# Optimization experiments

Measured on AMD Instinct MI355X. Metric: run time of the kernel, lower is better.

## Reference

```python
import jax, jax.numpy as jnp
import numpy as np

L = 16384; ENC = 64; DMODEL = 256; DSTATE = 64; DCONV = 4; EXPAND = 2
NLAYERS = 3; NCLASSES = 11
DIN = EXPAND * DMODEL                 # 512
HEADDIM = 64
NHEADS = DIN // HEADDIM               # 8
DXBC = DIN + 2 * DSTATE               # 640 (ngroups=1)
DPROJ = 2 * DIN + 2 * DSTATE + NHEADS # 1160
NDIR = 6
ORDERS = [(0, 1, 2), (0, 2, 1), (1, 0, 2), (1, 2, 0), (2, 0, 1), (2, 1, 0)]
SCALES = [1, 2, 4]
EPS = 1e-5


def setup_inputs() -> dict:
    key = jax.random.key(0)
    ks = iter(jax.random.split(key, 64))
    def nrm(shape, s=0.02):
        return jax.random.normal(next(ks), shape, jnp.float32) * s
    S = len(SCALES)
    return {
        "vec_real": jax.random.normal(next(ks), (L, ENC), jnp.float32),
        "vec_imag": jax.random.normal(next(ks), (L, ENC), jnp.float32),
        "coords": jax.random.randint(next(ks), (L, 4), 0, 128, jnp.int32),
        # input projection (Linear 128->256, LayerNorm)
        "inp_w": nrm((2 * ENC, DMODEL)), "inp_b": jnp.zeros((DMODEL,)),
        "inp_ln_w": jnp.ones((DMODEL,)), "inp_ln_b": jnp.zeros((DMODEL,)),
        # shared Mamba2 blocks, stacked over NLAYERS
        "ln_w": jnp.ones((NLAYERS, DMODEL)), "ln_b": jnp.zeros((NLAYERS, DMODEL)),
        "in_proj_w": nrm((NLAYERS, DMODEL, DPROJ)),
        "conv_w": nrm((NLAYERS, DXBC, DCONV), 0.1), "conv_b": jnp.zeros((NLAYERS, DXBC)),
        "dt_bias": nrm((NLAYERS, NHEADS), 0.5),
        "A_log": jnp.log(jnp.broadcast_to(jnp.arange(1, NHEADS + 1, dtype=jnp.float32), (NLAYERS, NHEADS))),
        "Dskip": jnp.ones((NLAYERS, NHEADS)),
        "rms_w": jnp.ones((NLAYERS, DIN)),
        "out_proj_w": nrm((NLAYERS, DIN, DMODEL)),
        # fusion MLP
        "fus_ln_w": jnp.ones((NDIR * DMODEL,)), "fus_ln_b": jnp.zeros((NDIR * DMODEL,)),
        "fus_w": nrm((NDIR * DMODEL, DMODEL)), "fus_b": jnp.zeros((DMODEL,)),
        # classifier
        "cls_ln_w": jnp.ones((S * DMODEL,)), "cls_ln_b": jnp.zeros((S * DMODEL,)),
        "cls_w1": nrm((S * DMODEL, 2 * DMODEL)), "cls_b1": jnp.zeros((2 * DMODEL,)),
        "cls_w2": nrm((2 * DMODEL, DMODEL)), "cls_b2": jnp.zeros((DMODEL,)),
        "cls_w3": nrm((DMODEL, NCLASSES)), "cls_b3": jnp.zeros((NCLASSES,)),
    }


def layer_norm(x, w, b):
    mu = x.mean(-1, keepdims=True)
    v = ((x - mu) ** 2).mean(-1, keepdims=True)
    return (x - mu) * jax.lax.rsqrt(v + EPS) * w + b


def mamba2(x, in_proj_w, conv_w, conv_b, dt_bias, A_log, Dskip, rms_w, out_proj_w):
    # x: [B, L, DMODEL]
    Bsz, Ls, _ = x.shape
    zxbcdt = x @ in_proj_w                                  # [B,L,DPROJ]
    z, xBC, dt = jnp.split(zxbcdt, [DIN, DIN + DXBC], axis=-1)
    dt = jax.nn.softplus(dt + dt_bias)                      # [B,L,H]
    # causal depthwise conv1d over xBC, then SiLU
    xc = jnp.transpose(xBC, (0, 2, 1))                      # [B,C,L]
    xc = jax.lax.conv_general_dilated(xc, conv_w[:, None, :], (1,), [(DCONV - 1, 0)],
                                      feature_group_count=DXBC)
    xBC = jax.nn.silu(jnp.transpose(xc, (0, 2, 1)) + conv_b)
    xs, Bm, Cm = jnp.split(xBC, [DIN, DIN + DSTATE], axis=-1)
    xs = xs.reshape(Bsz, Ls, NHEADS, HEADDIM)               # [B,L,H,P]
    A = -jnp.exp(A_log)                                     # [H]

    def step(state, inp):
        x_t, B_t, C_t, dt_t = inp                           # [B,H,P],[B,S],[B,S],[B,H]
        dA = jnp.exp(dt_t * A)                              # [B,H]
        state = state * dA[..., None, None] + (dt_t[..., None, None]
                 * x_t[..., :, None] * B_t[:, None, None, :])
        y = jnp.einsum('bhps,bs->bhp', state, C_t)
        return state, y

    init = jnp.zeros((Bsz, NHEADS, HEADDIM, DSTATE), x.dtype)
    seq = (jnp.moveaxis(xs, 1, 0), jnp.moveaxis(Bm, 1, 0),
           jnp.moveaxis(Cm, 1, 0), jnp.moveaxis(dt, 1, 0))
    _, ys = jax.lax.scan(step, init, seq)                   # [L,B,H,P]
    y = jnp.moveaxis(ys, 0, 1) + Dskip[None, None, :, None] * xs
    y = y.reshape(Bsz, Ls, DIN)
    # gated RMSNorm (norm_before_gate=False)
    y = y * jax.nn.silu(z)
    y = y * jax.lax.rsqrt((y * y).mean(-1, keepdims=True) + EPS) * rms_w
    return y @ out_proj_w


def reference(vec_real, vec_imag, coords, inp_w, inp_b, inp_ln_w, inp_ln_b,
              ln_w, ln_b, in_proj_w, conv_w, conv_b, dt_bias, A_log, Dskip,
              rms_w, out_proj_w, fus_ln_w, fus_ln_b, fus_w, fus_b,
              cls_ln_w, cls_ln_b, cls_w1, cls_b1, cls_w2, cls_b2, cls_w3, cls_b3):
    x = jnp.concatenate([vec_real, vec_imag], -1)           # [L,128]
    h = layer_norm(x @ inp_w + inp_b, inp_ln_w, inp_ln_b)
    h = jax.nn.gelu(h, approximate=False)                   # [L,D]
    # 6 traversal orders via lexsort (np.lexsort semantics: last key primary)
    perms = [jnp.lexsort(tuple(coords[:, a] for a in reversed(axes))) for axes in ORDERS]
    perm = jnp.stack(perms)                                 # [6,L]
    inv = jnp.argsort(perm, axis=1)                         # [6,L]
    xs = h[perm]                                            # [6,L,D] (directions as batch, shared weights)

    def layer_step(xcur, p):
        lw, lb, ipw, cw, cb, dtb, al, dk, rw, ow = p
        y = mamba2(layer_norm(xcur, lw, lb), ipw, cw, cb, dtb, al, dk, rw, ow)
        return xcur + y, None

    params = (ln_w, ln_b, in_proj_w, conv_w, conv_b, dt_bias, A_log, Dskip, rms_w, out_proj_w)
    xs, _ = jax.lax.scan(layer_step, xs, params)
    restored = jnp.take_along_axis(xs, inv[:, :, None], axis=1)  # [6,L,D]
    multi = jnp.transpose(restored, (1, 0, 2)).reshape(L, NDIR * DMODEL)
    fused = layer_norm(multi, fus_ln_w, fus_ln_b) @ fus_w + fus_b
    fused = jax.nn.gelu(fused, approximate=False)           # [L,D]
    # multi-scale pooling; L divisible by every scale -> equal windows
    pooled = jnp.concatenate([fused.reshape(s, L // s, DMODEL).mean(1).mean(0)
                              for s in SCALES], 0)          # [3*D]
    hc = layer_norm(pooled, cls_ln_w, cls_ln_b)
    hc = jax.nn.gelu(hc @ cls_w1 + cls_b1, approximate=False)
    hc = jax.nn.gelu(hc @ cls_w2 + cls_b2, approximate=False)
    return hc @ cls_w3 + cls_b3                             # [NCLASSES]
```

## Files before the change

### kernel.cpp

```cpp
#include <hip/hip_runtime.h>
#include <hip/hip_bf16.h>
#include <math.h>

#define LSEQ 16384
#define NC 128

using short8  = __attribute__((ext_vector_type(8))) short;
using floatx4 = __attribute__((ext_vector_type(4))) float;

__device__ __forceinline__ float bf2f(ushort u){ union{unsigned u; float f;} x; x.u = ((unsigned)u)<<16; return x.f; }
__device__ __forceinline__ ushort f2bf(float f){ union{float f; unsigned u;} x; x.f=f; unsigned u=x.u; return (ushort)((u + 0x7FFFu + ((u>>16)&1u)) >> 16); }
__device__ __forceinline__ float geluf(float x){ return 0.5f*x*(1.f+erff(x*0.70710678118654752f)); }
__device__ __forceinline__ float siluf(float x){ return x/(1.f+__expf(-x)); }
__device__ __forceinline__ float softplusf(float x){ return x>20.f ? x : log1pf(__expf(x)); }

__device__ __forceinline__ float blockSum256(float v, float* red){
  int t = threadIdx.x;
  red[t]=v; __syncthreads();
  #pragma unroll
  for (int s=128;s>0;s>>=1){ if (t<s) red[t]+=red[t+s]; __syncthreads(); }
  float r = red[0]; __syncthreads();
  return r;
}

__device__ const int ORD[6][3] = {{0,1,2},{0,2,1},{1,0,2},{1,2,0},{2,0,1},{2,1,0}};

__global__ __launch_bounds__(256) void sort_k(const int* __restrict__ coords, int* __restrict__ perm, int* __restrict__ inv){
  __shared__ unsigned long long sk[256];
  int d = blockIdx.y; int tid = threadIdx.x;
  int a0=ORD[d][0], a1=ORD[d][1], a2=ORD[d][2];
  int ibase = blockIdx.x*1024;
  unsigned long long mykey[4]; int rank[4] = {0,0,0,0};
  #pragma unroll
  for (int r=0;r<4;++r){
    int i = ibase + r*256 + tid;
    unsigned k3 = ((unsigned)coords[i*4+a0]<<14) | ((unsigned)coords[i*4+a1]<<7) | (unsigned)coords[i*4+a2];
    mykey[r] = (((unsigned long long)k3)<<14) | (unsigned)i;
  }
  for (int j0=0; j0<LSEQ; j0+=256){
    int j = j0 + tid;
    unsigned j3 = ((unsigned)coords[j*4+a0]<<14) | ((unsigned)coords[j*4+a1]<<7) | (unsigned)coords[j*4+a2];
    sk[tid] = (((unsigned long long)j3)<<14) | (unsigned)j;
    __syncthreads();
    #pragma unroll 8
    for (int jj=0; jj<256; ++jj){
      unsigned long long kj = sk[jj];
      #pragma unroll
      for (int r=0;r<4;++r) rank[r] += (kj < mykey[r]) ? 1 : 0;
    }
    __syncthreads();
  }
  #pragma unroll
  for (int r=0;r<4;++r){
    int i = ibase + r*256 + tid;
    perm[d*LSEQ + rank[r]] = i;
    inv[d*LSEQ + i] = rank[r];
  }
}

__global__ __launch_bounds__(256) void concat_k(const float* __restrict__ vr, const float* __restrict__ vi, float* __restrict__ xcat){
  int idx = blockIdx.x*256 + threadIdx.x;
  int i = idx >> 7, c = idx & 127;
  xcat[idx] = (c<64) ? vr[(i<<6)+c] : vi[(i<<6)+c-64];
}

__global__ __launch_bounds__(256) void tr_k(const float* __restrict__ in, ushort* __restrict__ out, int K, int N){
  __shared__ float tile[32][33];
  int tx = threadIdx.x & 31, ty = threadIdx.x >> 5;
  int k0 = blockIdx.y*32, n0 = blockIdx.x*32;
  #pragma unroll
  for (int q=0;q<4;++q){
    int k = k0 + ty + q*8, n = n0 + tx;
    if (k < K && n < N) tile[ty+q*8][tx] = in[(size_t)k*N + n];
  }
  __syncthreads();
  #pragma unroll
  for (int q=0;q<4;++q){
    int n = n0 + ty + q*8, k = k0 + tx;
    if (n < N && k < K) out[(size_t)n*K + k] = f2bf(tile[tx][ty+q*8]);
  }
}

template<int EPI, bool AF32>
__global__ __launch_bounds__(256) void gemm_bf_k(
  const void* __restrict__ Ain, int lda, const ushort* __restrict__ Bt,
  int N, int K, float* __restrict__ of,
  const float* __restrict__ bias, const float* __restrict__ rrow)
{
  __shared__ __align__(16) ushort As[64*32];
  __shared__ __align__(16) ushort Bs[64*32];
  int tid = threadIdx.x;
  int n0 = blockIdx.x*64, m0 = blockIdx.y*64;
  int w = tid>>6, lane = tid&63;
  int wm = (w>>1)*32, wn = (w&1)*32;
  int sr = tid>>2, skk = (tid&3)*8;
  floatx4 acc[2][2] = {};
  for (int k0=0; k0<K; k0+=32){
    if constexpr (AF32){
      const float* A = (const float*)Ain;
      float4 v0 = *(const float4*)(A + (size_t)(m0+sr)*lda + k0 + skk);
      float4 v1 = *(const float4*)(A + (size_t)(m0+sr)*lda + k0 + skk + 4);
      ushort o[8] = {f2bf(v0.x),f2bf(v0.y),f2bf(v0.z),f2bf(v0.w),f2bf(v1.x),f2bf(v1.y),f2bf(v1.z),f2bf(v1.w)};
      *(uint4*)(&As[sr*32+skk]) = *(uint4*)o;
    } else {
      const ushort* A = (const ushort*)Ain;
      *(uint4*)(&As[sr*32+skk]) = *(const uint4*)(A + (size_t)(m0+sr)*lda + k0 + skk);
    }
    uint4 bv = make_uint4(0u,0u,0u,0u);
    if (n0+sr < N) bv = *(const uint4*)(Bt + (size_t)(n0+sr)*K + k0 + skk);
    *(uint4*)(&Bs[sr*32+skk]) = bv;
    __syncthreads();
    int kq = lane>>4, l16 = lane&15;
    short8 bf0 = *(const short8*)(&Bs[(wn      + l16)*32 + kq*8]);
    short8 bf1 = *(const short8*)(&Bs[(wn + 16 + l16)*32 + kq*8]);
    #pragma unroll
    for (int ti=0; ti<2; ++ti){
      short8 af = *(const short8*)(&As[(wm + ti*16 + l16)*32 + kq*8]);
      acc[ti][0] = __builtin_amdgcn_mfma_f32_16x16x32_bf16(af, bf0, acc[ti][0], 0,0,0);
      acc[ti][1] = __builtin_amdgcn_mfma_f32_16x16x32_bf16(af, bf1, acc[ti][1], 0,0,0);
    }
    __syncthreads();
  }
  int l16 = lane&15, lq = lane>>4;
  #pragma unroll
  for (int ti=0; ti<2; ++ti)
  #pragma unroll
  for (int tj=0; tj<2; ++tj)
  #pragma unroll
  for (int r=0; r<4; ++r){
    int row = m0 + wm + ti*16 + lq*4 + r;
    int col = n0 + wn + tj*16 + l16;
    if (col >= N) continue;
    float v = acc[ti][tj][r];
    if (EPI==0){ of[(size_t)row*N + col] = v + bias[col]; }
    else if (EPI==2){ of[(size_t)row*N + col] += v * rrow[row]; }
    else { of[(size_t)row*N + col] = geluf(v + bias[col]); }
  }
}

__global__ __launch_bounds__(256) void gemm1_k(
  const float* __restrict__ xs,
  const float* __restrict__ lnw, const float* __restrict__ lnb,
  const ushort* __restrict__ Wt,
  ushort* __restrict__ xbc, float* __restrict__ odt, const float* __restrict__ dtb)
{
  __shared__ __align__(16) ushort As[64*264];
  __shared__ __align__(16) ushort Bs[64*32];
  int tid = threadIdx.x;
  int m0 = blockIdx.x*64;
  int w = tid>>6, lane = tid&63;
  int wm = (w>>1)*32, wn = (w&1)*32;
  int sr = tid>>2, skk = (tid&3)*8;
  int l16 = lane&15, kq = lane>>4;
  float va[8][8];
  float s = 0.f, s2 = 0.f;
  const float* rowp = xs + (size_t)(m0+sr)*256;
  #pragma unroll
  for (int ki=0;ki<8;++ki){
    float4 v0 = *(const float4*)(rowp + ki*32 + skk);
    float4 v1 = *(const float4*)(rowp + ki*32 + skk + 4);
    va[ki][0]=v0.x; va[ki][1]=v0.y; va[ki][2]=v0.z; va[ki][3]=v0.w;
    va[ki][4]=v1.x; va[ki][5]=v1.y; va[ki][6]=v1.z; va[ki][7]=v1.w;
    #pragma unroll
    for (int j=0;j<8;++j){ s += va[ki][j]; s2 += va[ki][j]*va[ki][j]; }
  }
  s  += __shfl_xor(s,1,64);  s  += __shfl_xor(s,2,64);
  s2 += __shfl_xor(s2,1,64); s2 += __shfl_xor(s2,2,64);
  float mu = s*(1.f/256.f);
  float var = s2*(1.f/256.f) - mu*mu;
  float rs = rsqrtf(fmaxf(var,0.f)+1e-5f);
  #pragma unroll
  for (int ki=0;ki<8;++ki){
    ushort o[8];
    #pragma unroll
    for (int j=0;j<8;++j) o[j] = f2bf((va[ki][j]-mu)*rs*lnw[ki*32+skk+j] + lnb[ki*32+skk+j]);
    *(uint4*)(&As[sr*264 + ki*32 + skk]) = *(uint4*)o;
  }
  __syncthreads();
  for (int nt=0; nt<11; ++nt){
    floatx4 acc[2][2] = {};
    for (int k0=0; k0<256; k0+=32){
      int nr = 512 + nt*64 + sr;
      uint4 bv = make_uint4(0u,0u,0u,0u);
      if (nr < 1160) bv = *(const uint4*)(Wt + (size_t)nr*256 + k0 + skk);
      *(uint4*)(&Bs[sr*32+skk]) = bv;
      __syncthreads();
      short8 bf0 = *(const short8*)(&Bs[(wn      + l16)*32 + kq*8]);
      short8 bf1 = *(const short8*)(&Bs[(wn + 16 + l16)*32 + kq*8]);
      #pragma unroll
      for (int ti=0; ti<2; ++ti){
        short8 af = *(const short8*)(&As[(wm + ti*16 + l16)*264 + k0 + kq*8]);
        acc[ti][0] = __builtin_amdgcn_mfma_f32_16x16x32_bf16(af, bf0, acc[ti][0], 0,0,0);
        acc[ti][1] = __builtin_amdgcn_mfma_f32_16x16x32_bf16(af, bf1, acc[ti][1], 0,0,0);
      }
      __syncthreads();
    }
    #pragma unroll
    for (int ti=0; ti<2; ++ti)
    #pragma unroll
    for (int tj=0; tj<2; ++tj)
    #pragma unroll
    for (int r=0; r<4; ++r){
      int row = m0 + wm + ti*16 + kq*4 + r;
      int col = nt*64 + wn + tj*16 + l16;
      float v = acc[ti][tj][r];
      if (col < 640) xbc[(size_t)row*640 + col] = f2bf(v);
      else if (col < 648) odt[(size_t)row*8 + (col-640)] = softplusf(v + dtb[col-640]);
    }
  }
}

__global__ __launch_bounds__(256) void ln_gelu_k(const float* __restrict__ in, float* __restrict__ out,
    const float* __restrict__ w, const float* __restrict__ b){
  __shared__ float red[256];
  int t = threadIdx.x; size_t base = (size_t)blockIdx.x*256;
  float v = in[base+t];
  float mu = blockSum256(v, red) * (1.f/256.f);
  float dv = v - mu;
  float var = blockSum256(dv*dv, red) * (1.f/256.f);
  float rs = rsqrtf(var + 1e-5f);
  out[base+t] = geluf(dv*rs*w[t] + b[t]);
}

__global__ __launch_bounds__(256) void scatter_k(const float* __restrict__ h, const int* __restrict__ perm, float* __restrict__ xs){
  int blk = blockIdx.x;
  int t = threadIdx.x;
  int d = blk >> 14; int r = blk & 16383;
  int src = perm[d*LSEQ + r];
  xs[(size_t)blk*256 + t] = h[(size_t)src*256 + t];
}

__global__ __launch_bounds__(256) void bnd_k(const ushort* __restrict__ xbc, ushort* __restrict__ bnd){
  int b = blockIdx.x;
  int d = b / NC, c = b % NC;
  size_t row0 = (size_t)d*LSEQ + (size_t)c*128;
  for (int idx = threadIdx.x; idx < 3*640; idx += 256){
    int j = idx/640;
    ushort v = (c==0) ? (ushort)0 : xbc[(row0 - 3 + j)*640 + (idx - j*640)];
    bnd[(size_t)b*3*640 + idx] = v;
  }
}

__global__ __launch_bounds__(256) void conv_k(ushort* __restrict__ xbc, const ushort* __restrict__ bnd,
    const float* __restrict__ convw, const float* __restrict__ convb){
  int b = blockIdx.x;
  int d = b / NC, c = b % NC;
  size_t row0 = (size_t)d*LSEQ + (size_t)c*128;
  int tid = threadIdx.x;
  for (int s0 = tid; s0 < 640; s0 += 256){
    float w0=convw[s0*4], w1=convw[s0*4+1], w2=convw[s0*4+2], w3=convw[s0*4+3];
    float cb=convb[s0];
    float h0=0.f,h1=0.f,h2=0.f;
    if (c != 0){
      const ushort* bp = bnd + (size_t)b*3*640;
      h0=bf2f(bp[s0]); h1=bf2f(bp[640+s0]); h2=bf2f(bp[1280+s0]);
    }
    ushort* p = xbc + row0*640 + s0;
    for (int r=0;r<128;++r){
      float cur = bf2f(*p);
      *p = f2bf(siluf(cb + w0*h0 + w1*h1 + w2*h2 + w3*cur));
      h0=h1; h1=h2; h2=cur;
      p += 640;
    }
  }
}

__global__ __launch_bounds__(256) void ssd_dstate_k(
  const ushort* __restrict__ xbc, const float* __restrict__ dtf, const float* __restrict__ alog,
  ushort* __restrict__ dsb, float* __restrict__ gam, int dh0)
{
  int c = blockIdx.x, dhg = blockIdx.y;
  int dh = dh0 + dhg;
  int d = dh >> 3, h = dh & 7;
  int tid = threadIdx.x;
  float Ah = -__expf(alog[h]);
  __shared__ __align__(16) ushort XT[64*136];
  __shared__ __align__(16) ushort BwT[64*136];
  __shared__ float sdt[128];
  __shared__ float scs[128];
  size_t row0 = (size_t)d*LSEQ + (size_t)c*128;
  if (tid < 128){
    float v = dtf[(row0+tid)*8 + h];
    sdt[tid] = v;
    float x = v;
    #pragma unroll
    for (int o=1;o<64;o<<=1){ float t = __shfl_up(x,(unsigned)o,64); if ((tid&63)>=o) x += t; }
    scs[tid] = x;
  }
  __syncthreads();
  if (tid>=64 && tid<128) scs[tid] += scs[63];
  __syncthreads();
  float csLast = scs[127];
  if (tid == 0) gam[(size_t)dh*NC + c] = __expf(Ah*csLast);
  for (int idx = tid; idx < 128*16; idx += 256){
    int s = idx >> 4, g = idx & 15;
    int ch = (g<8) ? h*64 + g*8 : 512 + (g-8)*8;
    uint4 v = *(const uint4*)(xbc + (row0+s)*640 + ch);
    ushort u[8]; *(uint4*)u = v;
    if (g < 8){
      int c0 = g*8;
      #pragma unroll
      for (int j=0;j<8;++j) XT[(c0+j)*136 + s] = u[j];
    } else {
      float wgt = __expf(Ah*(csLast - scs[s])) * sdt[s];
      int n0 = (g-8)*8;
      #pragma unroll
      for (int j=0;j<8;++j) BwT[(n0+j)*136 + s] = f2bf(bf2f(u[j])*wgt);
    }
  }
  __syncthreads();
  int w = tid>>6, lane = tid&63, l16 = lane&15, kq = lane>>4;
  floatx4 acc[4] = {};
  #pragma unroll
  for (int kw=0; kw<4; ++kw){
    short8 bfrag = *(const short8*)(&BwT[(16*w + l16)*136 + kw*32 + kq*8]);
    #pragma unroll
    for (int mt=0; mt<4; ++mt){
      short8 afrag = *(const short8*)(&XT[(mt*16 + l16)*136 + kw*32 + kq*8]);
      acc[mt] = __builtin_amdgcn_mfma_f32_16x16x32_bf16(afrag, bfrag, acc[mt], 0,0,0);
    }
  }
  size_t base = ((size_t)dhg*NC + c)*4096;
  int n = 16*w + l16;
  int kb = n>>5, nm = n&31;
  #pragma unroll
  for (int mt=0; mt<4; ++mt)
  #pragma unroll
  for (int r=0; r<4; ++r){
    int p = mt*16 + kq*4 + r;
    dsb[base + (size_t)kb*2048 + p*32 + nm] = f2bf(acc[mt][r]);
  }
}

__global__ __launch_bounds__(256) void ssd_scan_k(ushort* __restrict__ dsb, const float* __restrict__ gam, int dh0)
{
  int dhg = blockIdx.x;
  int tid = threadIdx.x;
  float S[16];
  #pragma unroll
  for (int j=0;j<16;++j) S[j]=0.f;
  int p = tid>>2, q = tid&3;
  size_t off16 = (size_t)(q>>1)*2048 + p*32 + (q&1)*16;
  ushort* base = dsb + (size_t)dhg*NC*4096 + off16;
  const float* g = gam + (size_t)(dh0+dhg)*NC;
  uint4 pf[4][2];
  #pragma unroll
  for (int j=0;j<4;++j){
    pf[j][0] = *(const uint4*)(base + (size_t)j*4096);
    pf[j][1] = *(const uint4*)(base + (size_t)j*4096 + 8);
  }
  for (int c=0;c<NC;++c){
    ushort cur[16];
    *(uint4*)(cur)   = pf[c&3][0];
    *(uint4*)(cur+8) = pf[c&3][1];
    if (c+4 < NC){
      pf[c&3][0] = *(const uint4*)(base + (size_t)(c+4)*4096);
      pf[c&3][1] = *(const uint4*)(base + (size_t)(c+4)*4096 + 8);
    }
    float gamma = g[c];
    ushort pfo[16];
    #pragma unroll
    for (int j=0;j<16;++j) pfo[j] = f2bf(S[j]);
    *(uint4*)(base + (size_t)c*4096)     = *(uint4*)(pfo);
    *(uint4*)(base + (size_t)c*4096 + 8) = *(uint4*)(pfo+8);
    #pragma unroll
    for (int j=0;j<16;++j) S[j] = gamma*S[j] + bf2f(cur[j]);
  }
}

__global__ __launch_bounds__(256) void ssd_out_k(
  ushort* __restrict__ xbc, const ushort* __restrict__ dsb,
  const float* __restrict__ dtf, const float* __restrict__ alog, const float* __restrict__ dskip, int dh0)
{
  int c = blockIdx.x, dhg = blockIdx.y;
  int dh = dh0 + dhg;
  int d = dh>>3, h = dh&7;
  int tid = threadIdx.x;
  float Ah = -__expf(alog[h]);
  float Dv = dskip[h];
  __shared__ __align__(16) ushort Cs[2][128][32];
  __shared__ __align__(16) ushort Bs2[2][128][32];
  __shared__ __align__(16) ushort XT[64*136];
  __shared__ __align__(16) ushort Pl[4][32*32];
  __shared__ float sdt[128];
  __shared__ float scs[128];
  size_t row0 = (size_t)d*LSEQ + (size_t)c*128;
  if (tid < 128){
    float v = dtf[(row0+tid)*8 + h];
    sdt[tid] = v;
    float x = v;
    #pragma unroll
    for (int o=1;o<64;o<<=1){ float t = __shfl_up(x,(unsigned)o,64); if ((tid&63)>=o) x += t; }
    scs[tid] = x;
  }
  __syncthreads();
  if (tid>=64 && tid<128) scs[tid] += scs[63];
  __syncthreads();
  for (int idx = tid; idx < 128*24; idx += 256){
    int s = idx/24, g = idx - s*24;
    int ch = (g<8) ? h*64 + g*8 : 512 + (g-8)*8;
    uint4 v = *(const uint4*)(xbc + (row0+s)*640 + ch);
    ushort u[8]; *(uint4*)u = v;
    if (g < 8){
      int c0 = g*8;
      #pragma unroll
      for (int j=0;j<8;++j) XT[(c0+j)*136 + s] = u[j];
    } else if (g < 16){
      int n0 = (g-8)*8;
      #pragma unroll
      for (int j=0;j<8;++j) Bs2[(n0+j)>>5][s][(n0+j)&31] = u[j];
    } else {
      int n0 = (g-16)*8;
      #pragma unroll
      for (int j=0;j<8;++j) Cs[(n0+j)>>5][s][(n0+j)&31] = u[j];
    }
  }
  int w = tid>>6, lane = tid&63, l16 = lane&15, kq = lane>>4;
  size_t pbase = ((size_t)dhg*NC + c)*4096;
  short8 sinf[4][2];
  #pragma unroll
  for (int nt=0; nt<4; ++nt)
  #pragma unroll
  for (int kb=0; kb<2; ++kb)
    sinf[nt][kb] = *(const short8*)(dsb + pbase + (size_t)kb*2048 + (nt*16+l16)*32 + kq*8);
  __syncthreads();
  short8 cfr[2][2];
  #pragma unroll
  for (int mt=0; mt<2; ++mt)
  #pragma unroll
  for (int kb=0; kb<2; ++kb)
    cfr[mt][kb] = *(const short8*)(&Cs[kb][w*32 + mt*16 + l16][kq*8]);
  floatx4 Y[2][4] = {};
  #pragma unroll
  for (int mt=0; mt<2; ++mt)
  #pragma unroll
  for (int nt=0; nt<4; ++nt)
  #pragma unroll
  for (int kb=0; kb<2; ++kb)
    Y[mt][nt] = __builtin_amdgcn_mfma_f32_16x16x32_bf16(cfr[mt][kb], sinf[nt][kb], Y[mt][nt], 0,0,0);
  #pragma unroll
  for (int mt=0; mt<2; ++mt){
    float ar[4];
    #pragma unroll
    for (int r=0;r<4;++r) ar[r] = __expf(Ah*scs[w*32 + mt*16 + kq*4 + r]);
    #pragma unroll
    for (int nt=0; nt<4; ++nt)
    #pragma unroll
    for (int r=0;r<4;++r) Y[mt][nt][r] *= ar[r];
  }
  for (int st=0; st<=w; ++st){
    floatx4 P[2][2] = {};
    #pragma unroll
    for (int nt2=0; nt2<2; ++nt2)
    #pragma unroll
    for (int kb=0; kb<2; ++kb){
      short8 bfr = *(const short8*)(&Bs2[kb][st*32 + nt2*16 + l16][kq*8]);
      #pragma unroll
      for (int mt=0; mt<2; ++mt)
        P[mt][nt2] = __builtin_amdgcn_mfma_f32_16x16x32_bf16(cfr[mt][kb], bfr, P[mt][nt2], 0,0,0);
    }
    #pragma unroll
    for (int mt=0; mt<2; ++mt)
    #pragma unroll
    for (int nt2=0; nt2<2; ++nt2)
    #pragma unroll
    for (int r=0; r<4; ++r){
      int tl = w*32 + mt*16 + kq*4 + r;
      int sl = st*32 + nt2*16 + l16;
      float e = __expf(fminf(Ah*(scs[tl]-scs[sl]), 0.f)) * sdt[sl];
      float v = (sl <= tl) ? P[mt][nt2][r]*e : 0.f;
      Pl[w][(mt*16 + kq*4 + r)*32 + nt2*16 + l16] = f2bf(v);
    }
    #pragma unroll
    for (int mt=0; mt<2; ++mt){
      short8 afr = *(const short8*)(&Pl[w][(mt*16 + l16)*32 + kq*8]);
      #pragma unroll
      for (int nt=0; nt<4; ++nt){
        short8 xfr = *(const short8*)(&XT[(nt*16 + l16)*136 + st*32 + kq*8]);
        Y[mt][nt] = __builtin_amdgcn_mfma_f32_16x16x32_bf16(afr, xfr, Y[mt][nt], 0,0,0);
      }
    }
  }
  #pragma unroll
  for (int mt=0; mt<2; ++mt)
  #pragma unroll
  for (int nt=0; nt<4; ++nt)
  #pragma unroll
  for (int r=0; r<4; ++r){
    int tl = w*32 + mt*16 + kq*4 + r;
    int p  = nt*16 + l16;
    float xv = bf2f(XT[p*136 + tl]);
    float yv = Y[mt][nt][r] + Dv*xv;
    xbc[(row0 + tl)*640 + h*64 + p] = f2bf(yv);
  }
}

__global__ __launch_bounds__(512) void scan_legacy_k(ushort* __restrict__ xbc, const float* __restrict__ dtf,
  const float* __restrict__ convw, const float* __restrict__ convb,
  const float* __restrict__ alog, const float* __restrict__ dskip)
{
  int d = blockIdx.x >> 3, h = blockIdx.x & 7;
  int tid = threadIdx.x, p = tid & 63, sg = tid >> 6;
  float Ah = -__expf(alog[h]);
  float Dv = dskip[h];
  __shared__ float raw[19][192];
  __shared__ float cw[192][4];
  __shared__ float cb[192];
  __shared__ float sxc[16][192];
  __shared__ float sdt[16];
  __shared__ float sy[16][8][64];
  for (int c = tid; c < 192; c += 512){
    int ch = (c<64) ? h*64+c : (c<128 ? 512+(c-64) : 576+(c-128));
    #pragma unroll
    for (int k=0;k<4;++k) cw[c][k] = convw[ch*4+k];
    cb[c] = convb[ch];
  }
  for (int idx = tid; idx < 3*192; idx += 512) raw[idx/192][idx%192] = 0.f;
  float st[8];
  #pragma unroll
  for (int j=0;j<8;++j) st[j]=0.f;
  size_t rowbase = (size_t)d*LSEQ;
  __syncthreads();
  for (int t0=0; t0<LSEQ; t0+=16){
    for (int idx = tid; idx < 16*192; idx += 512){
      int tt = idx/192, c = idx%192;
      int ch = (c<64) ? h*64+c : (c<128 ? 512+(c-64) : 576+(c-128));
      raw[3+tt][c] = bf2f(xbc[(rowbase + t0 + tt)*640 + ch]);
    }
    if (tid < 16) sdt[tid] = dtf[(rowbase + t0 + tid)*8 + h];
    __syncthreads();
    for (int idx = tid; idx < 16*192; idx += 512){
      int tt = idx/192, c = idx%192;
      float v = cb[c] + cw[c][0]*raw[tt][c] + cw[c][1]*raw[tt+1][c]
                      + cw[c][2]*raw[tt+2][c] + cw[c][3]*raw[tt+3][c];
      sxc[tt][c] = siluf(v);
    }
    __syncthreads();
    for (int tt=0; tt<16; ++tt){
      float dtv = sdt[tt];
      float dA = __expf(dtv*Ah);
      float xb = dtv * sxc[tt][p];
      float Bl[8], Cl[8];
      #pragma unroll
      for (int q=0;q<2;++q){
        *(floatx4*)&Bl[q*4] = *(const floatx4*)&sxc[tt][64  + sg*8 + q*4];
        *(floatx4*)&Cl[q*4] = *(const floatx4*)&sxc[tt][128 + sg*8 + q*4];
      }
      float part = 0.f;
      #pragma unroll
      for (int j=0;j<8;++j){ st[j] = st[j]*dA + xb*Bl[j]; part += st[j]*Cl[j]; }
      sy[tt][sg][p] = part;
    }
    __syncthreads();
    for (int idx = tid; idx < 16*64; idx += 512){
      int tt = idx>>6, pp = idx&63;
      float yv = sy[tt][0][pp]+sy[tt][1][pp]+sy[tt][2][pp]+sy[tt][3][pp]
               + sy[tt][4][pp]+sy[tt][5][pp]+sy[tt][6][pp]+sy[tt][7][pp] + Dv*sxc[tt][pp];
      xbc[(rowbase + t0 + tt)*640 + h*64 + pp] = f2bf(yv);
    }
    for (int idx = tid; idx < 3*192; idx += 512){
      int r = idx/192, c = idx%192;
      raw[r][c] = raw[16+r][c];
    }
    __syncthreads();
  }
}

__global__ __launch_bounds__(256) void zgate_k(
  const float* __restrict__ xs,
  const float* __restrict__ lnw, const float* __restrict__ lnb,
  const ushort* __restrict__ Wzt, ushort* __restrict__ xbc,
  const float* __restrict__ rmsw, float* __restrict__ rrg)
{
  __shared__ __align__(16) ushort As[64*264];
  __shared__ __align__(16) ushort Bs[64*32];
  __shared__ float gsum[64*32];
  int tid = threadIdx.x;
  int m0 = blockIdx.x*64;
  int w = tid>>6, lane = tid&63;
  int wm = (w>>1)*32, wn = (w&1)*32;
  int sr = tid>>2, skk = (tid&3)*8;
  int l16 = lane&15, kq = lane>>4;
  float va[8][8];
  float s = 0.f, s2 = 0.f;
  const float* rowp = xs + (size_t)(m0+sr)*256;
  #pragma unroll
  for (int ki=0;ki<8;++ki){
    float4 v0 = *(const float4*)(rowp + ki*32 + skk);
    float4 v1 = *(const float4*)(rowp + ki*32 + skk + 4);
    va[ki][0]=v0.x; va[ki][1]=v0.y; va[ki][2]=v0.z; va[ki][3]=v0.w;
    va[ki][4]=v1.x; va[ki][5]=v1.y; va[ki][6]=v1.z; va[ki][7]=v1.w;
    #pragma unroll
    for (int j=0;j<8;++j){ s += va[ki][j]; s2 += va[ki][j]*va[ki][j]; }
  }
  s  += __shfl_xor(s,1,64);  s  += __shfl_xor(s,2,64);
  s2 += __shfl_xor(s2,1,64); s2 += __shfl_xor(s2,2,64);
  float mu = s*(1.f/256.f);
  float var = s2*(1.f/256.f) - mu*mu;
  float rs = rsqrtf(fmaxf(var,0.f)+1e-5f);
  #pragma unroll
  for (int ki=0;ki<8;++ki){
    ushort o[8];
    #pragma unroll
    for (int j=0;j<8;++j) o[j] = f2bf((va[ki][j]-mu)*rs*lnw[ki*32+skk+j] + lnb[ki*32+skk+j]);
    *(uint4*)(&As[sr*264 + ki*32 + skk]) = *(uint4*)o;
  }
  float racc[2][4] = {};
  __syncthreads();
  for (int nt=0; nt<8; ++nt){
    floatx4 acc[2][2] = {};
    for (int k0=0; k0<256; k0+=32){
      uint4 bv = *(const uint4*)(Wzt + (size_t)(nt*64 + sr)*256 + k0 + skk);
      *(uint4*)(&Bs[sr*32+skk]) = bv;
      __syncthreads();
      short8 bf0 = *(const short8*)(&Bs[(wn      + l16)*32 + kq*8]);
      short8 bf1 = *(const short8*)(&Bs[(wn + 16 + l16)*32 + kq*8]);
      #pragma unroll
      for (int ti=0; ti<2; ++ti){
        short8 af = *(const short8*)(&As[(wm + ti*16 + l16)*264 + k0 + kq*8]);
        acc[ti][0] = __builtin_amdgcn_mfma_f32_16x16x32_bf16(af, bf0, acc[ti][0], 0,0,0);
        acc[ti][1] = __builtin_amdgcn_mfma_f32_16x16x32_bf16(af, bf1, acc[ti][1], 0,0,0);
      }
      __syncthreads();
    }
    #pragma unroll
    for (int ti=0; ti<2; ++ti)
    #pragma unroll
    for (int tj=0; tj<2; ++tj)
    #pragma unroll
    for (int r=0; r<4; ++r){
      int row = m0 + wm + ti*16 + kq*4 + r;
      int col = nt*64 + wn + tj*16 + l16;
      float z = acc[ti][tj][r];
      float y = bf2f(xbc[(size_t)row*640 + col]);
      float g = y * siluf(z);
      racc[ti][r] += g*g;
      xbc[(size_t)row*640 + col] = f2bf(g * rmsw[col]);
    }
  }
  #pragma unroll
  for (int ti=0; ti<2; ++ti)
  #pragma unroll
  for (int r=0; r<4; ++r)
    gsum[(wm + ti*16 + kq*4 + r)*32 + (w&1)*16 + l16] = racc[ti][r];
  __syncthreads();
  if (tid < 64){
    float s0 = 0.f;
    #pragma unroll 8
    for (int cc=0;cc<32;++cc) s0 += gsum[tid*32+cc];
    rrg[m0+tid] = rsqrtf(s0*(1.f/512.f) + 1e-5f);
  }
}

__global__ __launch_bounds__(256) void fuse_ln_k(const float* __restrict__ xs, const int* __restrict__ inv,
    const float* __restrict__ w, const float* __restrict__ b, float* __restrict__ out){
  __shared__ float red[256];
  int i = blockIdx.x, t = threadIdx.x;
  float v[6];
  float s = 0.f;
  #pragma unroll
  for (int d=0; d<6; ++d){
    int r = inv[d*LSEQ + i];
    v[d] = xs[((size_t)d*LSEQ + r)*256 + t];
    s += v[d];
  }
  float mu = blockSum256(s, red) * (1.f/1536.f);
  float s2 = 0.f;
  #pragma unroll
  for (int d=0; d<6; ++d){ float dv = v[d]-mu; s2 += dv*dv; }
  float var = blockSum256(s2, red) * (1.f/1536.f);
  float rs = rsqrtf(var + 1e-5f);
  #pragma unroll
  for (int d=0; d<6; ++d){
    int c = d*256 + t;
    out[(size_t)i*1536 + c] = (v[d]-mu)*rs*w[c] + b[c];
  }
}

__global__ void zero_k(float* p){ p[threadIdx.x] = 0.f; }

__global__ __launch_bounds__(256) void pool_k(const float* __restrict__ fused, float* __restrict__ pooled){
  int t = threadIdx.x;
  size_t r0 = (size_t)blockIdx.x*256;
  float s = 0.f;
  for (int r=0;r<256;++r) s += fused[(r0+r)*256 + t];
  atomicAdd(&pooled[t], s);
}

__global__ __launch_bounds__(256) void cls_k(const float* __restrict__ pooled,
  const float* __restrict__ lnw, const float* __restrict__ lnb,
  const float* __restrict__ w1, const float* __restrict__ b1,
  const float* __restrict__ w2, const float* __restrict__ b2,
  const float* __restrict__ w3, const float* __restrict__ b3, float* __restrict__ out)
{
  __shared__ float red[256];
  __shared__ float hcn[768]; __shared__ float h1[512]; __shared__ float h2[256];
  int t = threadIdx.x;
  float m = pooled[t] * (1.f/16384.f);
  float mu = blockSum256(m, red) * (1.f/256.f);
  float dv = m - mu;
  float var = blockSum256(dv*dv, red) * (1.f/256.f);
  float rs = rsqrtf(var + 1e-5f);
  #pragma unroll
  for (int rep=0; rep<3; ++rep){
    int c = rep*256 + t;
    hcn[c] = dv*rs*lnw[c] + lnb[c];
  }
  __syncthreads();
  for (int n=t; n<512; n+=256){
    float a = b1[n];
    for (int c=0;c<768;++c) a += hcn[c]*w1[c*512+n];
    h1[n] = geluf(a);
  }
  __syncthreads();
  {
    float a = b2[t];
    for (int c=0;c<512;++c) a += h1[c]*w2[c*256+t];
    h2[t] = geluf(a);
  }
  __syncthreads();
  if (t<11){
    float a = b3[t];
    for (int c=0;c<256;++c) a += h2[c]*w3[c*11+t];
    out[t] = a;
  }
}

extern "C" void kernel_launch(void* const* d_in, const int* in_sizes, int n_in,
                              void* d_out, int out_size, void* d_ws, size_t ws_size,
                              hipStream_t stream)
{
  const float* vec_real = (const float*)d_in[0];
  const float* vec_imag = (const float*)d_in[1];
  const int*   coords   = (const int*)d_in[2];
  const float* inp_w    = (const float*)d_in[3];
  const float* inp_b    = (const float*)d_in[4];
  const float* inp_ln_w = (const float*)d_in[5];
  const float* inp_ln_b = (const float*)d_in[6];
  const float* ln_w     = (const float*)d_in[7];
  const float* ln_b     = (const float*)d_in[8];
  const float* in_proj_w= (const float*)d_in[9];
  const float* conv_w   = (const float*)d_in[10];
  const float* conv_b   = (const float*)d_in[11];
  const float* dt_bias  = (const float*)d_in[12];
  const float* A_log    = (const float*)d_in[13];
  const float* Dskip    = (const float*)d_in[14];
  const float* rms_w    = (const float*)d_in[15];
  const float* out_proj_w=(const float*)d_in[16];
  const float* fus_ln_w = (const float*)d_in[17];
  const float* fus_ln_b = (const float*)d_in[18];
  const float* fus_w    = (const float*)d_in[19];
  const float* fus_b    = (const float*)d_in[20];
  const float* cls_ln_w = (const float*)d_in[21];
  const float* cls_ln_b = (const float*)d_in[22];
  const float* cls_w1   = (const float*)d_in[23];
  const float* cls_b1   = (const float*)d_in[24];
  const float* cls_w2   = (const float*)d_in[25];
  const float* cls_b2   = (const float*)d_in[26];
  const float* cls_w3   = (const float*)d_in[27];
  const float* cls_b3   = (const float*)d_in[28];
  (void)in_sizes; (void)n_in; (void)out_size;

  char* ws = (char*)d_ws;
  size_t off = 0;
  auto alloc = [&](size_t bytes)->char* { char* p = ws + off; off = (off + bytes + 255) & ~(size_t)255; return p; };
  int*    perm  = (int*)alloc((size_t)6*LSEQ*4);
  int*    inv   = (int*)alloc((size_t)6*LSEQ*4);
  float*  xs    = (float*)alloc((size_t)6*LSEQ*256*4);
  ushort* xbc   = (ushort*)alloc((size_t)6*LSEQ*640*2);
  float*  dtfb  = (float*)alloc((size_t)6*LSEQ*8*4);
  float*  rrg   = (float*)alloc((size_t)6*LSEQ*4);
  ushort* wtr   = (ushort*)alloc((size_t)1536*256*2);
  float*  pooled= (float*)alloc(256*4);
  size_t base_off = off;
  if (base_off > ws_size) return;

  float* gam = (float*)((char*)wtr + 600*1024);

  const size_t BND_SZ = (size_t)6*NC*3*640*2;
  size_t dsb_off = base_off + ((BND_SZ + 255) & ~(size_t)255);
  ushort* bndb = (ushort*)(ws + base_off);
  ushort* dsb  = (ushort*)(ws + dsb_off);
  long long avail2 = (long long)ws_size - (long long)dsb_off;
  int gsize = 0;
  const int cands[10] = {48,24,16,12,8,6,4,3,2,1};
  for (int ci=0; ci<10; ++ci){
    if ((long long)((size_t)cands[ci]*NC*4096*2 + 512) <= avail2){ gsize = cands[ci]; break; }
  }

  float* xcat = (float*)((char*)xbc + 0);
  float* tmpF = (float*)((char*)xbc + (16u<<20));
  float* hbuf = (float*)((char*)xbc + (48u<<20));
  float* multiF = (float*)((char*)xbc + 0);
  float* fused  = (float*)((char*)xbc + (100u<<20));

  dim3 b256(256);
  sort_k<<<dim3(16,6),b256,0,stream>>>(coords, perm, inv);
  concat_k<<<dim3(LSEQ*128/256),b256,0,stream>>>(vec_real, vec_imag, xcat);
  tr_k<<<dim3(8,4),b256,0,stream>>>(inp_w, wtr, 128, 256);
  gemm_bf_k<0,true><<<dim3(4, LSEQ/64),b256,0,stream>>>(xcat, 128, wtr, 256, 128, tmpF, inp_b, nullptr);
  ln_gelu_k<<<dim3(LSEQ),b256,0,stream>>>(tmpF, hbuf, inp_ln_w, inp_ln_b);
  scatter_k<<<dim3(6*LSEQ),b256,0,stream>>>(hbuf, perm, xs);

  for (int l=0;l<3;++l){
    const float* cwp = conv_w + (size_t)l*640*4;
    const float* cbp = conv_b + (size_t)l*640;
    const float* alp = A_log + l*8;
    const float* dkp = Dskip + l*8;
    tr_k<<<dim3(37,8),b256,0,stream>>>(in_proj_w + (size_t)l*256*1160, wtr, 256, 1160);
    gemm1_k<<<dim3(6*LSEQ/64),b256,0,stream>>>(xs, ln_w + l*256, ln_b + l*256,
        wtr, xbc, dtfb, dt_bias + l*8);
    if (gsize > 0){
      bnd_k<<<dim3(6*NC),b256,0,stream>>>(xbc, bndb);
      conv_k<<<dim3(6*NC),b256,0,stream>>>(xbc, bndb, cwp, cbp);
      for (int dh0=0; dh0<48; dh0+=gsize){
        ssd_dstate_k<<<dim3(NC,gsize),b256,0,stream>>>(xbc, dtfb, alp, dsb, gam, dh0);
        ssd_scan_k<<<dim3(gsize),b256,0,stream>>>(dsb, gam, dh0);
        ssd_out_k<<<dim3(NC,gsize),b256,0,stream>>>(xbc, dsb, dtfb, alp, dkp, dh0);
      }
    } else {
      scan_legacy_k<<<dim3(48),dim3(512),0,stream>>>(xbc, dtfb, cwp, cbp, alp, dkp);
    }
    zgate_k<<<dim3(6*LSEQ/64),b256,0,stream>>>(xs, ln_w + l*256, ln_b + l*256,
        wtr, xbc, rms_w + l*512, rrg);
    tr_k<<<dim3(8,16),b256,0,stream>>>(out_proj_w + (size_t)l*512*256, wtr, 512, 256);
    gemm_bf_k<2,false><<<dim3(4, 6*LSEQ/64),b256,0,stream>>>(xbc, 640, wtr, 256, 512, xs, nullptr, rrg);
  }

  fuse_ln_k<<<dim3(LSEQ),b256,0,stream>>>(xs, inv, fus_ln_w, fus_ln_b, multiF);
  tr_k<<<dim3(8,48),b256,0,stream>>>(fus_w, wtr, 1536, 256);
  gemm_bf_k<3,true><<<dim3(4, LSEQ/64),b256,0,stream>>>(multiF, 1536, wtr, 256, 1536, fused, fus_b, nullptr);
  zero_k<<<dim3(1),b256,0,stream>>>(pooled);
  pool_k<<<dim3(64),b256,0,stream>>>(fused, pooled);
  cls_k<<<dim3(1),b256,0,stream>>>(pooled, cls_ln_w, cls_ln_b, cls_w1, cls_b1, cls_w2, cls_b2, cls_w3, cls_b3, (float*)d_out);
}
```

Before: 3.486 ms.

## Split sort ranking across blocks, widen scan grid, add full-N bf16 GEMM

The O(L^2) rank sort is split along the comparison dimension into four partial blocks per tile. Their counts are combined with atomics into a zeroed rank buffer, and a final kernel scatters perm and inv. The SSD chunk scan now launches twice as many blocks, each carrying half the state. A new GEMM computes all 256 output columns per block from an A tile staged once in LDS, and is used for the out_proj and fusion GEMMs. The fusion LayerNorm now writes bf16 so that GEMM reads half the bytes. The cost is extra launches, atomic traffic, and more accumulator registers per thread in the new GEMM.

```diff
diff --git a/kernel.cpp b/kernel.cpp
--- a/kernel.cpp
+++ b/kernel.cpp
@@ -25,19 +25,24 @@
 
 __device__ const int ORD[6][3] = {{0,1,2},{0,2,1},{1,0,2},{1,2,0},{2,0,1},{2,1,0}};
 
-__global__ __launch_bounds__(256) void sort_k(const int* __restrict__ coords, int* __restrict__ perm, int* __restrict__ inv){
+__global__ __launch_bounds__(256) void zrank_k(int* __restrict__ rank){
+  rank[blockIdx.x*256 + threadIdx.x] = 0;
+}
+
+__global__ __launch_bounds__(256) void sortp_k(const int* __restrict__ coords, int* __restrict__ rank){
   __shared__ unsigned long long sk[256];
   int d = blockIdx.y; int tid = threadIdx.x;
   int a0=ORD[d][0], a1=ORD[d][1], a2=ORD[d][2];
   int ibase = blockIdx.x*1024;
-  unsigned long long mykey[4]; int rank[4] = {0,0,0,0};
+  int jbase = blockIdx.z*4096;
+  unsigned long long mykey[4]; int rk[4] = {0,0,0,0};
   #pragma unroll
   for (int r=0;r<4;++r){
     int i = ibase + r*256 + tid;
     unsigned k3 = ((unsigned)coords[i*4+a0]<<14) | ((unsigned)coords[i*4+a1]<<7) | (unsigned)coords[i*4+a2];
     mykey[r] = (((unsigned long long)k3)<<14) | (unsigned)i;
   }
-  for (int j0=0; j0<LSEQ; j0+=256){
+  for (int j0=jbase; j0<jbase+4096; j0+=256){
     int j = j0 + tid;
     unsigned j3 = ((unsigned)coords[j*4+a0]<<14) | ((unsigned)coords[j*4+a1]<<7) | (unsigned)coords[j*4+a2];
     sk[tid] = (((unsigned long long)j3)<<14) | (unsigned)j;
@@ -46,16 +51,21 @@
     for (int jj=0; jj<256; ++jj){
       unsigned long long kj = sk[jj];
       #pragma unroll
-      for (int r=0;r<4;++r) rank[r] += (kj < mykey[r]) ? 1 : 0;
+      for (int r=0;r<4;++r) rk[r] += (kj < mykey[r]) ? 1 : 0;
     }
     __syncthreads();
   }
   #pragma unroll
-  for (int r=0;r<4;++r){
-    int i = ibase + r*256 + tid;
-    perm[d*LSEQ + rank[r]] = i;
-    inv[d*LSEQ + i] = rank[r];
-  }
+  for (int r=0;r<4;++r)
+    atomicAdd(&rank[d*LSEQ + ibase + r*256 + tid], rk[r]);
+}
+
+__global__ __launch_bounds__(256) void sfin_k(const int* __restrict__ rank, int* __restrict__ perm, int* __restrict__ inv){
+  int g = blockIdx.x*256 + threadIdx.x;
+  int d = g >> 14, i = g & 16383;
+  int r = rank[g];
+  perm[d*LSEQ + r] = i;
+  inv[g] = r;
 }
 
 __global__ __launch_bounds__(256) void concat_k(const float* __restrict__ vr, const float* __restrict__ vi, float* __restrict__ xcat){
@@ -132,9 +142,59 @@
     int col = n0 + wn + tj*16 + l16;
     if (col >= N) continue;
     float v = acc[ti][tj][r];
-    if (EPI==0){ of[(size_t)row*N + col] = v + bias[col]; }
-    else if (EPI==2){ of[(size_t)row*N + col] += v * rrow[row]; }
-    else { of[(size_t)row*N + col] = geluf(v + bias[col]); }
+    of[(size_t)row*N + col] = v + bias[col];
+  }
+}
+
+template<int KC, int EPI>
+__global__ __launch_bounds__(256) void gemmNS_k(
+  const ushort* __restrict__ A, int lda, const ushort* __restrict__ Bt,
+  float* __restrict__ of, const float* __restrict__ bias, const float* __restrict__ rrow)
+{
+  __shared__ __align__(16) ushort As[64*264];
+  __shared__ __align__(16) ushort Bs[64*32];
+  const int K = KC*256;
+  int tid = threadIdx.x;
+  int m0 = blockIdx.x*64;
+  int w = tid>>6, lane = tid&63;
+  int wm = (w>>1)*32, wn = (w&1)*32;
+  int sr = tid>>2, skk = (tid&3)*8;
+  int l16 = lane&15, kq = lane>>4;
+  floatx4 acc[4][2][2] = {};
+  for (int kb=0; kb<KC; ++kb){
+    #pragma unroll
+    for (int ki=0;ki<8;++ki)
+      *(uint4*)(&As[sr*264 + ki*32 + skk]) = *(const uint4*)(A + (size_t)(m0+sr)*lda + kb*256 + ki*32 + skk);
+    __syncthreads();
+    for (int nt=0; nt<4; ++nt){
+      for (int k0=0; k0<256; k0+=32){
+        *(uint4*)(&Bs[sr*32+skk]) = *(const uint4*)(Bt + (size_t)(nt*64+sr)*K + kb*256 + k0 + skk);
+        __syncthreads();
+        short8 bf0 = *(const short8*)(&Bs[(wn      + l16)*32 + kq*8]);
+        short8 bf1 = *(const short8*)(&Bs[(wn + 16 + l16)*32 + kq*8]);
+        #pragma unroll
+        for (int ti=0; ti<2; ++ti){
+          short8 af = *(const short8*)(&As[(wm + ti*16 + l16)*264 + k0 + kq*8]);
+          acc[nt][ti][0] = __builtin_amdgcn_mfma_f32_16x16x32_bf16(af, bf0, acc[nt][ti][0], 0,0,0);
+          acc[nt][ti][1] = __builtin_amdgcn_mfma_f32_16x16x32_bf16(af, bf1, acc[nt][ti][1], 0,0,0);
+        }
+        __syncthreads();
+      }
+    }
+  }
+  #pragma unroll
+  for (int nt=0; nt<4; ++nt)
+  #pragma unroll
+  for (int ti=0; ti<2; ++ti)
+  #pragma unroll
+  for (int tj=0; tj<2; ++tj)
+  #pragma unroll
+  for (int r=0; r<4; ++r){
+    int row = m0 + wm + ti*16 + kq*4 + r;
+    int col = nt*64 + wn + tj*16 + l16;
+    float v = acc[nt][ti][tj][r];
+    if (EPI==2) of[(size_t)row*256 + col] += v * rrow[row];
+    else        of[(size_t)row*256 + col] = geluf(v + bias[col]);
   }
 }
 
@@ -334,37 +394,27 @@
 
 __global__ __launch_bounds__(256) void ssd_scan_k(ushort* __restrict__ dsb, const float* __restrict__ gam, int dh0)
 {
-  int dhg = blockIdx.x;
+  int dhg = blockIdx.x, z = blockIdx.y;
   int tid = threadIdx.x;
-  float S[16];
-  #pragma unroll
-  for (int j=0;j<16;++j) S[j]=0.f;
-  int p = tid>>2, q = tid&3;
-  size_t off16 = (size_t)(q>>1)*2048 + p*32 + (q&1)*16;
-  ushort* base = dsb + (size_t)dhg*NC*4096 + off16;
+  float S[8];
+  #pragma unroll
+  for (int j=0;j<8;++j) S[j]=0.f;
+  ushort* base = dsb + (size_t)dhg*NC*4096 + (size_t)z*2048 + (size_t)(tid>>2)*32 + (size_t)(tid&3)*8;
   const float* g = gam + (size_t)(dh0+dhg)*NC;
-  uint4 pf[4][2];
-  #pragma unroll
-  for (int j=0;j<4;++j){
-    pf[j][0] = *(const uint4*)(base + (size_t)j*4096);
-    pf[j][1] = *(const uint4*)(base + (size_t)j*4096 + 8);
-  }
+  uint4 pf[4];
+  #pragma unroll
+  for (int j=0;j<4;++j) pf[j] = *(const uint4*)(base + (size_t)j*4096);
   for (int c=0;c<NC;++c){
-    ushort cur[16];
-    *(uint4*)(cur)   = pf[c&3][0];
-    *(uint4*)(cur+8) = pf[c&3][1];
-    if (c+4 < NC){
-      pf[c&3][0] = *(const uint4*)(base + (size_t)(c+4)*4096);
-      pf[c&3][1] = *(const uint4*)(base + (size_t)(c+4)*4096 + 8);
-    }
+    ushort cur[8];
+    *(uint4*)cur = pf[c&3];
+    if (c+4 < NC) pf[c&3] = *(const uint4*)(base + (size_t)(c+4)*4096);
     float gamma = g[c];
-    ushort pfo[16];
-    #pragma unroll
-    for (int j=0;j<16;++j) pfo[j] = f2bf(S[j]);
-    *(uint4*)(base + (size_t)c*4096)     = *(uint4*)(pfo);
-    *(uint4*)(base + (size_t)c*4096 + 8) = *(uint4*)(pfo+8);
-    #pragma unroll
-    for (int j=0;j<16;++j) S[j] = gamma*S[j] + bf2f(cur[j]);
+    ushort pfo[8];
+    #pragma unroll
+    for (int j=0;j<8;++j) pfo[j] = f2bf(S[j]);
+    *(uint4*)(base + (size_t)c*4096) = *(uint4*)pfo;
+    #pragma unroll
+    for (int j=0;j<8;++j) S[j] = gamma*S[j] + bf2f(cur[j]);
   }
 }
 
@@ -653,7 +703,7 @@
 }
 
 __global__ __launch_bounds__(256) void fuse_ln_k(const float* __restrict__ xs, const int* __restrict__ inv,
-    const float* __restrict__ w, const float* __restrict__ b, float* __restrict__ out){
+    const float* __restrict__ w, const float* __restrict__ b, ushort* __restrict__ out){
   __shared__ float red[256];
   int i = blockIdx.x, t = threadIdx.x;
   float v[6];
@@ -673,7 +723,7 @@
   #pragma unroll
   for (int d=0; d<6; ++d){
     int c = d*256 + t;
-    out[(size_t)i*1536 + c] = (v[d]-mu)*rs*w[c] + b[c];
+    out[(size_t)i*1536 + c] = f2bf((v[d]-mu)*rs*w[c] + b[c]);
   }
 }
 
@@ -776,6 +826,7 @@
   if (base_off > ws_size) return;
 
   float* gam = (float*)((char*)wtr + 600*1024);
+  int* rankb = (int*)rrg;
 
   const size_t BND_SZ = (size_t)6*NC*3*640*2;
   size_t dsb_off = base_off + ((BND_SZ + 255) & ~(size_t)255);
@@ -788,14 +839,16 @@
     if ((long long)((size_t)cands[ci]*NC*4096*2 + 512) <= avail2){ gsize = cands[ci]; break; }
   }
 
-  float* xcat = (float*)((char*)xbc + 0);
-  float* tmpF = (float*)((char*)xbc + (16u<<20));
-  float* hbuf = (float*)((char*)xbc + (48u<<20));
-  float* multiF = (float*)((char*)xbc + 0);
-  float* fused  = (float*)((char*)xbc + (100u<<20));
+  float*  xcat = (float*)((char*)xbc + 0);
+  float*  tmpF = (float*)((char*)xbc + (16u<<20));
+  float*  hbuf = (float*)((char*)xbc + (48u<<20));
+  ushort* multiB = (ushort*)((char*)xbc + 0);
+  float*  fused  = (float*)((char*)xbc + (100u<<20));
 
   dim3 b256(256);
-  sort_k<<<dim3(16,6),b256,0,stream>>>(coords, perm, inv);
+  zrank_k<<<dim3(6*LSEQ/256),b256,0,stream>>>(rankb);
+  sortp_k<<<dim3(16,6,4),b256,0,stream>>>(coords, rankb);
+  sfin_k<<<dim3(6*LSEQ/256),b256,0,stream>>>(rankb, perm, inv);
   concat_k<<<dim3(LSEQ*128/256),b256,0,stream>>>(vec_real, vec_imag, xcat);
   tr_k<<<dim3(8,4),b256,0,stream>>>(inp_w, wtr, 128, 256);
   gemm_bf_k<0,true><<<dim3(4, LSEQ/64),b256,0,stream>>>(xcat, 128, wtr, 256, 128, tmpF, inp_b, nullptr);
@@ -815,7 +868,7 @@
       conv_k<<<dim3(6*NC),b256,0,stream>>>(xbc, bndb, cwp, cbp);
       for (int dh0=0; dh0<48; dh0+=gsize){
         ssd_dstate_k<<<dim3(NC,gsize),b256,0,stream>>>(xbc, dtfb, alp, dsb, gam, dh0);
-        ssd_scan_k<<<dim3(gsize),b256,0,stream>>>(dsb, gam, dh0);
+        ssd_scan_k<<<dim3(gsize,2),b256,0,stream>>>(dsb, gam, dh0);
         ssd_out_k<<<dim3(NC,gsize),b256,0,stream>>>(xbc, dsb, dtfb, alp, dkp, dh0);
       }
     } else {
@@ -824,12 +877,12 @@
     zgate_k<<<dim3(6*LSEQ/64),b256,0,stream>>>(xs, ln_w + l*256, ln_b + l*256,
         wtr, xbc, rms_w + l*512, rrg);
     tr_k<<<dim3(8,16),b256,0,stream>>>(out_proj_w + (size_t)l*512*256, wtr, 512, 256);
-    gemm_bf_k<2,false><<<dim3(4, 6*LSEQ/64),b256,0,stream>>>(xbc, 640, wtr, 256, 512, xs, nullptr, rrg);
-  }
-
-  fuse_ln_k<<<dim3(LSEQ),b256,0,stream>>>(xs, inv, fus_ln_w, fus_ln_b, multiF);
+    gemmNS_k<2,2><<<dim3(6*LSEQ/64),b256,0,stream>>>(xbc, 640, wtr, xs, nullptr, rrg);
+  }
+
+  fuse_ln_k<<<dim3(LSEQ),b256,0,stream>>>(xs, inv, fus_ln_w, fus_ln_b, multiB);
   tr_k<<<dim3(8,48),b256,0,stream>>>(fus_w, wtr, 1536, 256);
-  gemm_bf_k<3,true><<<dim3(4, LSEQ/64),b256,0,stream>>>(multiF, 1536, wtr, 256, 1536, fused, fus_b, nullptr);
+  gemmNS_k<6,3><<<dim3(LSEQ/64),b256,0,stream>>>(multiB, 1536, wtr, fused, fus_b, nullptr);
   zero_k<<<dim3(1),b256,0,stream>>>(pooled);
   pool_k<<<dim3(64),b256,0,stream>>>(fused, pooled);
   cls_k<<<dim3(1),b256,0,stream>>>(pooled, cls_ln_w, cls_ln_b, cls_w1, cls_b1, cls_w2, cls_b2, cls_w3, cls_b3, (float*)d_out);
```

After: 3.119 ms. -10.5%, faster.
